# Kernel tuning notes

Hardware: AMD Instinct MI355X
Metric: run time of the kernel (lower is better)

Reference implementation:

```python
import jax, jax.numpy as jnp
import numpy as np

N = 100000      # hits
P = 512         # particle ids (0 = noise, skipped)
D = 8           # condensation-space dim
Q_MIN = 0.01
REPULSION_SCALING = 10.0


def setup_inputs() -> dict:
    key = jax.random.key(0)
    k1, k2, k3, k4, k5 = jax.random.split(key, 5)
    w = jax.random.normal(k1, (N,), dtype=jnp.float32)
    # beta in (0, 0.95) so arctanh stays well-conditioned
    beta = jax.random.uniform(k2, (N,), dtype=jnp.float32) * 0.95
    x = jax.random.normal(k3, (N, D), dtype=jnp.float32)
    y = jax.random.normal(k4, (N,), dtype=jnp.float32)
    particle_id = jax.random.randint(k5, (N,), 0, P)
    return {"w": w, "beta": beta, "x": x, "y": y, "particle_id": particle_id}


def _safe_sqrt(s):
    # sqrt with zero (sub)gradient at 0, matching torch.norm's behavior at 0
    pos = s > 0
    return jnp.where(pos, jnp.sqrt(jnp.where(pos, s, 1.0)), 0.0)


def _condensation_loss(beta, x, particle_id):
    n = beta.shape[0]
    q = jnp.arctanh(beta) ** 2 + Q_MIN                     # [N]
    # per-particle condensation point: hit with max q (torch.argmax -> first)
    q_max = jax.ops.segment_max(q, particle_id, num_segments=P)          # [P]
    counts = jax.ops.segment_sum(jnp.ones_like(q), particle_id, num_segments=P)
    is_max = q == q_max[particle_id]
    cand = jnp.where(is_max, jnp.arange(n), n)
    alpha_idx = jnp.clip(jax.ops.segment_min(cand, particle_id, num_segments=P), 0, n - 1)
    valid = (counts > 0) & (jnp.arange(P) != 0)            # skip noise pid 0 and absent pids
    q_alpha = jnp.where(valid, q_max, 0.0)                 # [P], sanitized (-inf for empty segs)
    x_alpha = x[alpha_idx]                                  # [P, D]
    # squared distances [N, P] via GEMM (avoids [N, P, D] intermediate)
    sq = (jnp.sum(x * x, axis=1, keepdims=True)
          - 2.0 * (x @ x_alpha.T)
          + jnp.sum(x_alpha * x_alpha, axis=1)[None, :])
    sq = jnp.maximum(sq, 0.0)
    dist = _safe_sqrt(sq)
    va = sq * q_alpha[None, :]                              # attractive potential
    vr = jnp.maximum(1.0 - dist, 0.0) * q_alpha[None, :]    # repulsive hinge
    M = (particle_id[:, None] == jnp.arange(P)[None, :]).astype(x.dtype)  # [N, P]
    per_p = jnp.mean(q[:, None] * (M * va + REPULSION_SCALING * (1.0 - M) * vr), axis=0)  # [P]
    return jnp.sum(jnp.where(valid, per_p, 0.0))


def reference(w, beta, x, y, particle_id):
    return _condensation_loss(beta, x, particle_id)
```

## Files before the change

kernel.cpp:

```cpp
#include <hip/hip_runtime.h>

#define P_IDS 512
#define DIM 8
#define QMIN 0.01f
#define REP 10.0f
#define CHUNK 64
#define NCHUNK (P_IDS / CHUNK)
#define HPT 4
#define HB (256 * HPT)

typedef unsigned long long ull;

__launch_bounds__(256)
__global__ void stageA_kernel(const float* __restrict__ beta,
                              const int* __restrict__ pid,
                              float* __restrict__ q_out,
                              ull* __restrict__ tables,
                              int n) {
    __shared__ ull s_keys[P_IDS];
    s_keys[threadIdx.x] = 0ULL;
    s_keys[threadIdx.x + 256] = 0ULL;
    __syncthreads();
    int i = blockIdx.x * 256 + threadIdx.x;
    if (i < n) {
        float b = beta[i];
        float at = 0.5f * logf((1.0f + b) / (1.0f - b));
        float qv = fmaf(at, at, QMIN);
        q_out[i] = qv;
        ull key = ((ull)__float_as_uint(qv) << 32) |
                  (ull)(unsigned int)(~(unsigned int)i);
        atomicMax(&s_keys[pid[i]], key);
    }
    __syncthreads();
    ull* dst = tables + (size_t)blockIdx.x * P_IDS;
    dst[threadIdx.x] = s_keys[threadIdx.x];
    dst[threadIdx.x + 256] = s_keys[threadIdx.x + 256];
}

__launch_bounds__(64)
__global__ void stageB_kernel(const ull* __restrict__ tables, int ntab,
                              const float* __restrict__ x,
                              float2* __restrict__ meta,
                              float* __restrict__ x_alpha,
                              float* __restrict__ out) {
    int p = blockIdx.x;
    ull k = 0ULL;
    for (int t = threadIdx.x; t < ntab; t += 64) {
        ull v = tables[(size_t)t * P_IDS + p];
        k = (v > k) ? v : k;
    }
#pragma unroll
    for (int off = 32; off > 0; off >>= 1) {
        ull o = __shfl_down(k, off, 64);
        k = (o > k) ? o : k;
    }
    if (threadIdx.x == 0) {
        bool valid = (k != 0ULL) && (p != 0);
        float qa = valid ? __uint_as_float((unsigned int)(k >> 32)) : 0.0f;
        int idx = valid ? (int)(~(unsigned int)(k & 0xFFFFFFFFull)) : 0;
        float4 a = ((const float4*)x)[idx * 2];
        float4 b = ((const float4*)x)[idx * 2 + 1];
        float xa2 = a.x * a.x;
        xa2 = fmaf(a.y, a.y, xa2); xa2 = fmaf(a.z, a.z, xa2); xa2 = fmaf(a.w, a.w, xa2);
        xa2 = fmaf(b.x, b.x, xa2); xa2 = fmaf(b.y, b.y, xa2); xa2 = fmaf(b.z, b.z, xa2);
        xa2 = fmaf(b.w, b.w, xa2);
        ((float4*)x_alpha)[p * 2] = a;
        ((float4*)x_alpha)[p * 2 + 1] = b;
        meta[p] = make_float2(qa, xa2);
        if (p == 0) out[0] = 0.0f;
    }
}

__launch_bounds__(256)
__global__ void loss_kernel(const float* __restrict__ x,
                            const float* __restrict__ q,
                            const int* __restrict__ pid,
                            const float2* __restrict__ meta,
                            const float* __restrict__ x_alpha,
                            float* __restrict__ out,
                            int n) {
    __shared__ float  s_xa[CHUNK * DIM];
    __shared__ float2 s_meta[CHUNK];
    int chunk = blockIdx.x & (NCHUNK - 1);
    int hb    = blockIdx.x / NCHUNK;
    int p0    = chunk * CHUNK;
    if (threadIdx.x < CHUNK * DIM / 4)
        ((float4*)s_xa)[threadIdx.x] =
            ((const float4*)(x_alpha + p0 * DIM))[threadIdx.x];
    if (threadIdx.x < CHUNK) s_meta[threadIdx.x] = meta[p0 + threadIdx.x];
    __syncthreads();

    float xi[HPT][DIM], xi2[HPT], qi[HPT], acc[HPT];
    int   myj[HPT];
    int base = hb * HB + threadIdx.x;
#pragma unroll
    for (int h = 0; h < HPT; ++h) {
        int i = base + h * 256;
        bool act = i < n;
        int ii = act ? i : 0;
        float4 v0 = ((const float4*)x)[ii * 2];
        float4 v1 = ((const float4*)x)[ii * 2 + 1];
        xi[h][0] = v0.x; xi[h][1] = v0.y; xi[h][2] = v0.z; xi[h][3] = v0.w;
        xi[h][4] = v1.x; xi[h][5] = v1.y; xi[h][6] = v1.z; xi[h][7] = v1.w;
        float s = 0.0f;
#pragma unroll
        for (int d = 0; d < DIM; ++d) s = fmaf(xi[h][d], xi[h][d], s);
        xi2[h] = s;
        qi[h]  = act ? q[ii] : 0.0f;
        myj[h] = act ? (pid[ii] - p0) : -1;
        acc[h] = 0.0f;
    }

    for (int j = 0; j < CHUNK; ++j) {
        float2 m  = s_meta[j];
        float4 a0 = ((const float4*)s_xa)[j * 2];
        float4 a1 = ((const float4*)s_xa)[j * 2 + 1];
        float sq[HPT];
#pragma unroll
        for (int h = 0; h < HPT; ++h) {
            float dot = xi[h][0] * a0.x;
            dot = fmaf(xi[h][1], a0.y, dot); dot = fmaf(xi[h][2], a0.z, dot);
            dot = fmaf(xi[h][3], a0.w, dot); dot = fmaf(xi[h][4], a1.x, dot);
            dot = fmaf(xi[h][5], a1.y, dot); dot = fmaf(xi[h][6], a1.z, dot);
            dot = fmaf(xi[h][7], a1.w, dot);
            sq[h] = fmaxf(fmaf(-2.0f, dot, xi2[h] + m.y), 0.0f);
        }
        float mn = fminf(fminf(sq[0], sq[1]), fminf(sq[2], sq[3]));
        if (__any(mn < 1.0f)) {
#pragma unroll
            for (int h = 0; h < HPT; ++h) {
                float vr = fmaxf(1.0f - __builtin_amdgcn_sqrtf(sq[h]), 0.0f);
                acc[h] = fmaf(vr, m.x, acc[h]);
            }
        }
    }

    float partial = 0.0f;
#pragma unroll
    for (int h = 0; h < HPT; ++h) {
        float t = REP * acc[h];
        int j = myj[h];
        if (j >= 0 && j < CHUNK) {
            float2 m = s_meta[j];
            float dot = xi[h][0] * s_xa[j * DIM + 0];
#pragma unroll
            for (int d = 1; d < DIM; ++d) dot = fmaf(xi[h][d], s_xa[j * DIM + d], dot);
            float sq = fmaxf(fmaf(-2.0f, dot, xi2[h] + m.y), 0.0f);
            float vr = fmaxf(1.0f - __builtin_amdgcn_sqrtf(sq), 0.0f);
            t += m.x * (sq - REP * vr);
        }
        partial = fmaf(qi[h], t, partial);
    }

#pragma unroll
    for (int off = 32; off > 0; off >>= 1)
        partial += __shfl_down(partial, off, 64);
    __shared__ float s_red[4];
    if ((threadIdx.x & 63) == 0) s_red[threadIdx.x >> 6] = partial;
    __syncthreads();
    if (threadIdx.x == 0)
        atomicAdd(out, (s_red[0] + s_red[1] + s_red[2] + s_red[3]) / (float)n);
}

extern "C" void kernel_launch(void* const* d_in, const int* in_sizes, int n_in,
                              void* d_out, int out_size, void* d_ws, size_t ws_size,
                              hipStream_t stream) {
    int n = in_sizes[0];
    const float* beta = (const float*)d_in[1];
    const float* x    = (const float*)d_in[2];
    const int*   pid  = (const int*)d_in[4];
    float* out = (float*)d_out;

    int a_blocks = (n + 255) / 256;
    char* ws = (char*)d_ws;
    size_t tab_bytes = (size_t)a_blocks * P_IDS * sizeof(ull);
    tab_bytes = (tab_bytes + 255) & ~(size_t)255;
    size_t q_bytes = (((size_t)n * 4) + 255) & ~(size_t)255;
    ull*    tables  = (ull*)ws;
    float*  q       = (float*)(ws + tab_bytes);
    float2* meta    = (float2*)(ws + tab_bytes + q_bytes);
    float*  x_alpha = (float*)(ws + tab_bytes + q_bytes + P_IDS * sizeof(float2));

    stageA_kernel<<<a_blocks, 256, 0, stream>>>(beta, pid, q, tables, n);
    stageB_kernel<<<P_IDS, 64, 0, stream>>>(tables, a_blocks, x, meta, x_alpha, out);
    int hit_blocks = (n + HB - 1) / HB;
    loss_kernel<<<hit_blocks * NCHUNK, 256, 0, stream>>>(x, q, pid, meta, x_alpha, out, n);
}
```

Measured before the change: 96.58 us.

## Fuse three stages into one cooperative kernel with grid-wide syncs

```diff
diff --git a/kernel.cpp b/kernel.cpp
--- a/kernel.cpp
+++ b/kernel.cpp
@@ -1,4 +1,7 @@
 #include <hip/hip_runtime.h>
+#include <hip/hip_cooperative_groups.h>
+
+namespace cg = cooperative_groups;
 
 #define P_IDS 512
 #define DIM 8
@@ -11,155 +14,164 @@
 
 typedef unsigned long long ull;
 
-__launch_bounds__(256)
-__global__ void stageA_kernel(const float* __restrict__ beta,
-                              const int* __restrict__ pid,
-                              float* __restrict__ q_out,
-                              ull* __restrict__ tables,
-                              int n) {
-    __shared__ ull s_keys[P_IDS];
-    s_keys[threadIdx.x] = 0ULL;
-    s_keys[threadIdx.x + 256] = 0ULL;
-    __syncthreads();
-    int i = blockIdx.x * 256 + threadIdx.x;
-    if (i < n) {
-        float b = beta[i];
-        float at = 0.5f * logf((1.0f + b) / (1.0f - b));
-        float qv = fmaf(at, at, QMIN);
-        q_out[i] = qv;
-        ull key = ((ull)__float_as_uint(qv) << 32) |
-                  (ull)(unsigned int)(~(unsigned int)i);
-        atomicMax(&s_keys[pid[i]], key);
-    }
-    __syncthreads();
-    ull* dst = tables + (size_t)blockIdx.x * P_IDS;
-    dst[threadIdx.x] = s_keys[threadIdx.x];
-    dst[threadIdx.x + 256] = s_keys[threadIdx.x + 256];
-}
-
-__launch_bounds__(64)
-__global__ void stageB_kernel(const ull* __restrict__ tables, int ntab,
-                              const float* __restrict__ x,
-                              float2* __restrict__ meta,
-                              float* __restrict__ x_alpha,
-                              float* __restrict__ out) {
-    int p = blockIdx.x;
-    ull k = 0ULL;
-    for (int t = threadIdx.x; t < ntab; t += 64) {
-        ull v = tables[(size_t)t * P_IDS + p];
-        k = (v > k) ? v : k;
-    }
-#pragma unroll
-    for (int off = 32; off > 0; off >>= 1) {
-        ull o = __shfl_down(k, off, 64);
-        k = (o > k) ? o : k;
-    }
-    if (threadIdx.x == 0) {
-        bool valid = (k != 0ULL) && (p != 0);
-        float qa = valid ? __uint_as_float((unsigned int)(k >> 32)) : 0.0f;
-        int idx = valid ? (int)(~(unsigned int)(k & 0xFFFFFFFFull)) : 0;
-        float4 a = ((const float4*)x)[idx * 2];
-        float4 b = ((const float4*)x)[idx * 2 + 1];
-        float xa2 = a.x * a.x;
-        xa2 = fmaf(a.y, a.y, xa2); xa2 = fmaf(a.z, a.z, xa2); xa2 = fmaf(a.w, a.w, xa2);
-        xa2 = fmaf(b.x, b.x, xa2); xa2 = fmaf(b.y, b.y, xa2); xa2 = fmaf(b.z, b.z, xa2);
-        xa2 = fmaf(b.w, b.w, xa2);
-        ((float4*)x_alpha)[p * 2] = a;
-        ((float4*)x_alpha)[p * 2 + 1] = b;
-        meta[p] = make_float2(qa, xa2);
-        if (p == 0) out[0] = 0.0f;
-    }
-}
-
-__launch_bounds__(256)
-__global__ void loss_kernel(const float* __restrict__ x,
-                            const float* __restrict__ q,
-                            const int* __restrict__ pid,
-                            const float2* __restrict__ meta,
-                            const float* __restrict__ x_alpha,
-                            float* __restrict__ out,
-                            int n) {
+__launch_bounds__(256, 4)
+__global__ void fused_kernel(const float* __restrict__ beta,
+                             const float* __restrict__ x,
+                             const int* __restrict__ pid,
+                             float* __restrict__ q,
+                             ull* __restrict__ tables,
+                             float2* __restrict__ meta,
+                             float* __restrict__ x_alpha,
+                             float* __restrict__ out,
+                             int n, int a_blocks, int tiles) {
+    cg::grid_group grid = cg::this_grid();
+    __shared__ ull    s_keys[P_IDS];
+    __shared__ ull    s_kred[4];
     __shared__ float  s_xa[CHUNK * DIM];
     __shared__ float2 s_meta[CHUNK];
-    int chunk = blockIdx.x & (NCHUNK - 1);
-    int hb    = blockIdx.x / NCHUNK;
-    int p0    = chunk * CHUNK;
-    if (threadIdx.x < CHUNK * DIM / 4)
-        ((float4*)s_xa)[threadIdx.x] =
-            ((const float4*)(x_alpha + p0 * DIM))[threadIdx.x];
-    if (threadIdx.x < CHUNK) s_meta[threadIdx.x] = meta[p0 + threadIdx.x];
-    __syncthreads();
-
-    float xi[HPT][DIM], xi2[HPT], qi[HPT], acc[HPT];
-    int   myj[HPT];
-    int base = hb * HB + threadIdx.x;
-#pragma unroll
-    for (int h = 0; h < HPT; ++h) {
-        int i = base + h * 256;
-        bool act = i < n;
-        int ii = act ? i : 0;
-        float4 v0 = ((const float4*)x)[ii * 2];
-        float4 v1 = ((const float4*)x)[ii * 2 + 1];
-        xi[h][0] = v0.x; xi[h][1] = v0.y; xi[h][2] = v0.z; xi[h][3] = v0.w;
-        xi[h][4] = v1.x; xi[h][5] = v1.y; xi[h][6] = v1.z; xi[h][7] = v1.w;
-        float s = 0.0f;
-#pragma unroll
-        for (int d = 0; d < DIM; ++d) s = fmaf(xi[h][d], xi[h][d], s);
-        xi2[h] = s;
-        qi[h]  = act ? q[ii] : 0.0f;
-        myj[h] = act ? (pid[ii] - p0) : -1;
-        acc[h] = 0.0f;
+    __shared__ float  s_red[4];
+
+    const int b   = blockIdx.x;
+    const int tid = threadIdx.x;
+
+    if (b < a_blocks) {
+        s_keys[tid] = 0ULL;
+        s_keys[tid + 256] = 0ULL;
+        __syncthreads();
+        int i = b * 256 + tid;
+        if (i < n) {
+            float bt = beta[i];
+            float at = 0.5f * logf((1.0f + bt) / (1.0f - bt));
+            float qv = fmaf(at, at, QMIN);
+            q[i] = qv;
+            ull key = ((ull)__float_as_uint(qv) << 32) |
+                      (ull)(unsigned int)(~(unsigned int)i);
+            atomicMax(&s_keys[pid[i]], key);
+        }
+        __syncthreads();
+        ull* dst = tables + (size_t)b * P_IDS;
+        dst[tid] = s_keys[tid];
+        dst[tid + 256] = s_keys[tid + 256];
     }
-
-    for (int j = 0; j < CHUNK; ++j) {
-        float2 m  = s_meta[j];
-        float4 a0 = ((const float4*)s_xa)[j * 2];
-        float4 a1 = ((const float4*)s_xa)[j * 2 + 1];
-        float sq[HPT];
+    grid.sync();
+
+    if (b < P_IDS) {
+        int p = b;
+        ull k = 0ULL;
+        for (int t = tid; t < a_blocks; t += 256) {
+            ull v = tables[(size_t)t * P_IDS + p];
+            k = (v > k) ? v : k;
+        }
+#pragma unroll
+        for (int off = 32; off > 0; off >>= 1) {
+            ull o = __shfl_down(k, off, 64);
+            k = (o > k) ? o : k;
+        }
+        if ((tid & 63) == 0) s_kred[tid >> 6] = k;
+        __syncthreads();
+        if (tid == 0) {
+            k = s_kred[0];
+            k = (s_kred[1] > k) ? s_kred[1] : k;
+            k = (s_kred[2] > k) ? s_kred[2] : k;
+            k = (s_kred[3] > k) ? s_kred[3] : k;
+            bool valid = (k != 0ULL) && (p != 0);
+            float qa = valid ? __uint_as_float((unsigned int)(k >> 32)) : 0.0f;
+            int idx = valid ? (int)(~(unsigned int)(k & 0xFFFFFFFFull)) : 0;
+            float4 a0 = ((const float4*)x)[idx * 2];
+            float4 a1 = ((const float4*)x)[idx * 2 + 1];
+            float xa2 = a0.x * a0.x;
+            xa2 = fmaf(a0.y, a0.y, xa2); xa2 = fmaf(a0.z, a0.z, xa2);
+            xa2 = fmaf(a0.w, a0.w, xa2); xa2 = fmaf(a1.x, a1.x, xa2);
+            xa2 = fmaf(a1.y, a1.y, xa2); xa2 = fmaf(a1.z, a1.z, xa2);
+            xa2 = fmaf(a1.w, a1.w, xa2);
+            ((float4*)x_alpha)[p * 2] = a0;
+            ((float4*)x_alpha)[p * 2 + 1] = a1;
+            meta[p] = make_float2(qa, xa2);
+            if (p == 0) out[0] = 0.0f;
+        }
+    }
+    grid.sync();
+
+    if (b < tiles) {
+        int chunk = b & (NCHUNK - 1);
+        int hb    = b / NCHUNK;
+        int p0    = chunk * CHUNK;
+        if (tid < CHUNK * DIM / 4)
+            ((float4*)s_xa)[tid] = ((const float4*)(x_alpha + p0 * DIM))[tid];
+        if (tid < CHUNK) s_meta[tid] = meta[p0 + tid];
+        __syncthreads();
+
+        float xi[HPT][DIM], xi2[HPT], qi[HPT], acc[HPT];
+        int   myj[HPT];
+        int base = hb * HB + tid;
 #pragma unroll
         for (int h = 0; h < HPT; ++h) {
-            float dot = xi[h][0] * a0.x;
-            dot = fmaf(xi[h][1], a0.y, dot); dot = fmaf(xi[h][2], a0.z, dot);
-            dot = fmaf(xi[h][3], a0.w, dot); dot = fmaf(xi[h][4], a1.x, dot);
-            dot = fmaf(xi[h][5], a1.y, dot); dot = fmaf(xi[h][6], a1.z, dot);
-            dot = fmaf(xi[h][7], a1.w, dot);
-            sq[h] = fmaxf(fmaf(-2.0f, dot, xi2[h] + m.y), 0.0f);
-        }
-        float mn = fminf(fminf(sq[0], sq[1]), fminf(sq[2], sq[3]));
-        if (__any(mn < 1.0f)) {
+            int i = base + h * 256;
+            bool act = i < n;
+            int ii = act ? i : 0;
+            float4 v0 = ((const float4*)x)[ii * 2];
+            float4 v1 = ((const float4*)x)[ii * 2 + 1];
+            xi[h][0] = v0.x; xi[h][1] = v0.y; xi[h][2] = v0.z; xi[h][3] = v0.w;
+            xi[h][4] = v1.x; xi[h][5] = v1.y; xi[h][6] = v1.z; xi[h][7] = v1.w;
+            float s = 0.0f;
+#pragma unroll
+            for (int d = 0; d < DIM; ++d) s = fmaf(xi[h][d], xi[h][d], s);
+            xi2[h] = s;
+            qi[h]  = act ? q[ii] : 0.0f;
+            myj[h] = act ? (pid[ii] - p0) : -1;
+            acc[h] = 0.0f;
+        }
+
+        for (int j = 0; j < CHUNK; ++j) {
+            float2 m  = s_meta[j];
+            float4 a0 = ((const float4*)s_xa)[j * 2];
+            float4 a1 = ((const float4*)s_xa)[j * 2 + 1];
+            float sq[HPT];
 #pragma unroll
             for (int h = 0; h < HPT; ++h) {
-                float vr = fmaxf(1.0f - __builtin_amdgcn_sqrtf(sq[h]), 0.0f);
-                acc[h] = fmaf(vr, m.x, acc[h]);
+                float dot = xi[h][0] * a0.x;
+                dot = fmaf(xi[h][1], a0.y, dot); dot = fmaf(xi[h][2], a0.z, dot);
+                dot = fmaf(xi[h][3], a0.w, dot); dot = fmaf(xi[h][4], a1.x, dot);
+                dot = fmaf(xi[h][5], a1.y, dot); dot = fmaf(xi[h][6], a1.z, dot);
+                dot = fmaf(xi[h][7], a1.w, dot);
+                sq[h] = fmaxf(fmaf(-2.0f, dot, xi2[h] + m.y), 0.0f);
             }
-        }
+            float mn = fminf(fminf(sq[0], sq[1]), fminf(sq[2], sq[3]));
+            if (__any(mn < 1.0f)) {
+#pragma unroll
+                for (int h = 0; h < HPT; ++h) {
+                    float vr = fmaxf(1.0f - __builtin_amdgcn_sqrtf(sq[h]), 0.0f);
+                    acc[h] = fmaf(vr, m.x, acc[h]);
+                }
+            }
+        }
+
+        float partial = 0.0f;
+#pragma unroll
+        for (int h = 0; h < HPT; ++h) {
+            float t = REP * acc[h];
+            int j = myj[h];
+            if (j >= 0 && j < CHUNK) {
+                float2 m = s_meta[j];
+                float dot = xi[h][0] * s_xa[j * DIM + 0];
+#pragma unroll
+                for (int d = 1; d < DIM; ++d)
+                    dot = fmaf(xi[h][d], s_xa[j * DIM + d], dot);
+                float sq = fmaxf(fmaf(-2.0f, dot, xi2[h] + m.y), 0.0f);
+                float vr = fmaxf(1.0f - __builtin_amdgcn_sqrtf(sq), 0.0f);
+                t += m.x * (sq - REP * vr);
+            }
+            partial = fmaf(qi[h], t, partial);
+        }
+
+#pragma unroll
+        for (int off = 32; off > 0; off >>= 1)
+            partial += __shfl_down(partial, off, 64);
+        if ((tid & 63) == 0) s_red[tid >> 6] = partial;
+        __syncthreads();
+        if (tid == 0)
+            atomicAdd(out, (s_red[0] + s_red[1] + s_red[2] + s_red[3]) / (float)n);
     }
-
-    float partial = 0.0f;
-#pragma unroll
-    for (int h = 0; h < HPT; ++h) {
-        float t = REP * acc[h];
-        int j = myj[h];
-        if (j >= 0 && j < CHUNK) {
-            float2 m = s_meta[j];
-            float dot = xi[h][0] * s_xa[j * DIM + 0];
-#pragma unroll
-            for (int d = 1; d < DIM; ++d) dot = fmaf(xi[h][d], s_xa[j * DIM + d], dot);
-            float sq = fmaxf(fmaf(-2.0f, dot, xi2[h] + m.y), 0.0f);
-            float vr = fmaxf(1.0f - __builtin_amdgcn_sqrtf(sq), 0.0f);
-            t += m.x * (sq - REP * vr);
-        }
-        partial = fmaf(qi[h], t, partial);
-    }
-
-#pragma unroll
-    for (int off = 32; off > 0; off >>= 1)
-        partial += __shfl_down(partial, off, 64);
-    __shared__ float s_red[4];
-    if ((threadIdx.x & 63) == 0) s_red[threadIdx.x >> 6] = partial;
-    __syncthreads();
-    if (threadIdx.x == 0)
-        atomicAdd(out, (s_red[0] + s_red[1] + s_red[2] + s_red[3]) / (float)n);
 }
 
 extern "C" void kernel_launch(void* const* d_in, const int* in_sizes, int n_in,
@@ -172,17 +184,21 @@
     float* out = (float*)d_out;
 
     int a_blocks = (n + 255) / 256;
+    int tiles    = ((n + HB - 1) / HB) * NCHUNK;
+    int grid     = tiles > P_IDS ? tiles : P_IDS;
+    if (grid < a_blocks) grid = a_blocks;
+
     char* ws = (char*)d_ws;
-    size_t tab_bytes = (size_t)a_blocks * P_IDS * sizeof(ull);
-    tab_bytes = (tab_bytes + 255) & ~(size_t)255;
-    size_t q_bytes = (((size_t)n * 4) + 255) & ~(size_t)255;
+    size_t tab_bytes = ((size_t)a_blocks * P_IDS * sizeof(ull) + 255) & ~(size_t)255;
+    size_t q_bytes   = (((size_t)n * 4) + 255) & ~(size_t)255;
     ull*    tables  = (ull*)ws;
     float*  q       = (float*)(ws + tab_bytes);
     float2* meta    = (float2*)(ws + tab_bytes + q_bytes);
     float*  x_alpha = (float*)(ws + tab_bytes + q_bytes + P_IDS * sizeof(float2));
 
-    stageA_kernel<<<a_blocks, 256, 0, stream>>>(beta, pid, q, tables, n);
-    stageB_kernel<<<P_IDS, 64, 0, stream>>>(tables, a_blocks, x, meta, x_alpha, out);
-    int hit_blocks = (n + HB - 1) / HB;
-    loss_kernel<<<hit_blocks * NCHUNK, 256, 0, stream>>>(x, q, pid, meta, x_alpha, out, n);
+    void* args[] = {(void*)&beta, (void*)&x, (void*)&pid, (void*)&q,
+                    (void*)&tables, (void*)&meta, (void*)&x_alpha, (void*)&out,
+                    (void*)&n, (void*)&a_blocks, (void*)&tiles};
+    hipLaunchCooperativeKernel((void*)fused_kernel, dim3(grid), dim3(256),
+                               args, 0, stream);
 }
```

Measured after the change: 285.7 us. 196% more time.

## Fold per-particle argmax reduction into loss kernel with fixed 64 partial tables

Applied to the files above, without the earlier changes.

```diff
diff --git a/kernel.cpp b/kernel.cpp
--- a/kernel.cpp
+++ b/kernel.cpp
@@ -4,6 +4,7 @@
 #define DIM 8
 #define QMIN 0.01f
 #define REP 10.0f
+#define TBLS 64
 #define CHUNK 64
 #define NCHUNK (P_IDS / CHUNK)
 #define HPT 4
@@ -16,13 +17,13 @@
                               const int* __restrict__ pid,
                               float* __restrict__ q_out,
                               ull* __restrict__ tables,
+                              float* __restrict__ out,
                               int n) {
     __shared__ ull s_keys[P_IDS];
     s_keys[threadIdx.x] = 0ULL;
     s_keys[threadIdx.x + 256] = 0ULL;
     __syncthreads();
-    int i = blockIdx.x * 256 + threadIdx.x;
-    if (i < n) {
+    for (int i = blockIdx.x * 256 + threadIdx.x; i < n; i += TBLS * 256) {
         float b = beta[i];
         float at = 0.5f * logf((1.0f + b) / (1.0f - b));
         float qv = fmaf(at, at, QMIN);
@@ -35,64 +36,58 @@
     ull* dst = tables + (size_t)blockIdx.x * P_IDS;
     dst[threadIdx.x] = s_keys[threadIdx.x];
     dst[threadIdx.x + 256] = s_keys[threadIdx.x + 256];
-}
-
-__launch_bounds__(64)
-__global__ void stageB_kernel(const ull* __restrict__ tables, int ntab,
-                              const float* __restrict__ x,
-                              float2* __restrict__ meta,
-                              float* __restrict__ x_alpha,
-                              float* __restrict__ out) {
-    int p = blockIdx.x;
-    ull k = 0ULL;
-    for (int t = threadIdx.x; t < ntab; t += 64) {
-        ull v = tables[(size_t)t * P_IDS + p];
-        k = (v > k) ? v : k;
-    }
-#pragma unroll
-    for (int off = 32; off > 0; off >>= 1) {
-        ull o = __shfl_down(k, off, 64);
-        k = (o > k) ? o : k;
-    }
-    if (threadIdx.x == 0) {
-        bool valid = (k != 0ULL) && (p != 0);
-        float qa = valid ? __uint_as_float((unsigned int)(k >> 32)) : 0.0f;
-        int idx = valid ? (int)(~(unsigned int)(k & 0xFFFFFFFFull)) : 0;
-        float4 a = ((const float4*)x)[idx * 2];
-        float4 b = ((const float4*)x)[idx * 2 + 1];
-        float xa2 = a.x * a.x;
-        xa2 = fmaf(a.y, a.y, xa2); xa2 = fmaf(a.z, a.z, xa2); xa2 = fmaf(a.w, a.w, xa2);
-        xa2 = fmaf(b.x, b.x, xa2); xa2 = fmaf(b.y, b.y, xa2); xa2 = fmaf(b.z, b.z, xa2);
-        xa2 = fmaf(b.w, b.w, xa2);
-        ((float4*)x_alpha)[p * 2] = a;
-        ((float4*)x_alpha)[p * 2 + 1] = b;
-        meta[p] = make_float2(qa, xa2);
-        if (p == 0) out[0] = 0.0f;
-    }
+    if (blockIdx.x == 0 && threadIdx.x == 0) out[0] = 0.0f;
 }
 
 __launch_bounds__(256)
 __global__ void loss_kernel(const float* __restrict__ x,
                             const float* __restrict__ q,
                             const int* __restrict__ pid,
-                            const float2* __restrict__ meta,
-                            const float* __restrict__ x_alpha,
+                            const ull* __restrict__ tables,
                             float* __restrict__ out,
                             int n) {
+    __shared__ ull    s_part[4][CHUNK];
     __shared__ float  s_xa[CHUNK * DIM];
     __shared__ float2 s_meta[CHUNK];
-    int chunk = blockIdx.x & (NCHUNK - 1);
-    int hb    = blockIdx.x / NCHUNK;
-    int p0    = chunk * CHUNK;
-    if (threadIdx.x < CHUNK * DIM / 4)
-        ((float4*)s_xa)[threadIdx.x] =
-            ((const float4*)(x_alpha + p0 * DIM))[threadIdx.x];
-    if (threadIdx.x < CHUNK) s_meta[threadIdx.x] = meta[p0 + threadIdx.x];
+    __shared__ float  s_red[4];
+
+    const int tid  = threadIdx.x;
+    const int wave = tid >> 6, lane = tid & 63;
+    const int chunk = blockIdx.x & (NCHUNK - 1);
+    const int hb    = blockIdx.x / NCHUNK;
+    const int p0    = chunk * CHUNK;
+
+    ull k = 0ULL;
+#pragma unroll
+    for (int t = wave; t < TBLS; t += 4) {
+        ull v = tables[(size_t)t * P_IDS + p0 + lane];
+        k = (v > k) ? v : k;
+    }
+    s_part[wave][lane] = k;
+    __syncthreads();
+    if (tid < CHUNK) {
+        k = s_part[0][tid];
+        ull v1 = s_part[1][tid], v2 = s_part[2][tid], v3 = s_part[3][tid];
+        k = (v1 > k) ? v1 : k; k = (v2 > k) ? v2 : k; k = (v3 > k) ? v3 : k;
+        bool valid = (k != 0ULL) && ((p0 + tid) != 0);
+        float qa = valid ? __uint_as_float((unsigned int)(k >> 32)) : 0.0f;
+        int idx = valid ? (int)(~(unsigned int)(k & 0xFFFFFFFFull)) : 0;
+        float4 a0 = ((const float4*)x)[idx * 2];
+        float4 a1 = ((const float4*)x)[idx * 2 + 1];
+        float xa2 = a0.x * a0.x;
+        xa2 = fmaf(a0.y, a0.y, xa2); xa2 = fmaf(a0.z, a0.z, xa2);
+        xa2 = fmaf(a0.w, a0.w, xa2); xa2 = fmaf(a1.x, a1.x, xa2);
+        xa2 = fmaf(a1.y, a1.y, xa2); xa2 = fmaf(a1.z, a1.z, xa2);
+        xa2 = fmaf(a1.w, a1.w, xa2);
+        ((float4*)s_xa)[tid * 2] = a0;
+        ((float4*)s_xa)[tid * 2 + 1] = a1;
+        s_meta[tid] = make_float2(qa, xa2);
+    }
     __syncthreads();
 
     float xi[HPT][DIM], xi2[HPT], qi[HPT], acc[HPT];
     int   myj[HPT];
-    int base = hb * HB + threadIdx.x;
+    int base = hb * HB + tid;
 #pragma unroll
     for (int h = 0; h < HPT; ++h) {
         int i = base + h * 256;
@@ -144,7 +139,8 @@
             float2 m = s_meta[j];
             float dot = xi[h][0] * s_xa[j * DIM + 0];
 #pragma unroll
-            for (int d = 1; d < DIM; ++d) dot = fmaf(xi[h][d], s_xa[j * DIM + d], dot);
+            for (int d = 1; d < DIM; ++d)
+                dot = fmaf(xi[h][d], s_xa[j * DIM + d], dot);
             float sq = fmaxf(fmaf(-2.0f, dot, xi2[h] + m.y), 0.0f);
             float vr = fmaxf(1.0f - __builtin_amdgcn_sqrtf(sq), 0.0f);
             t += m.x * (sq - REP * vr);
@@ -155,10 +151,9 @@
 #pragma unroll
     for (int off = 32; off > 0; off >>= 1)
         partial += __shfl_down(partial, off, 64);
-    __shared__ float s_red[4];
-    if ((threadIdx.x & 63) == 0) s_red[threadIdx.x >> 6] = partial;
+    if ((tid & 63) == 0) s_red[tid >> 6] = partial;
     __syncthreads();
-    if (threadIdx.x == 0)
+    if (tid == 0)
         atomicAdd(out, (s_red[0] + s_red[1] + s_red[2] + s_red[3]) / (float)n);
 }
 
@@ -171,18 +166,12 @@
     const int*   pid  = (const int*)d_in[4];
     float* out = (float*)d_out;
 
-    int a_blocks = (n + 255) / 256;
     char* ws = (char*)d_ws;
-    size_t tab_bytes = (size_t)a_blocks * P_IDS * sizeof(ull);
-    tab_bytes = (tab_bytes + 255) & ~(size_t)255;
-    size_t q_bytes = (((size_t)n * 4) + 255) & ~(size_t)255;
-    ull*    tables  = (ull*)ws;
-    float*  q       = (float*)(ws + tab_bytes);
-    float2* meta    = (float2*)(ws + tab_bytes + q_bytes);
-    float*  x_alpha = (float*)(ws + tab_bytes + q_bytes + P_IDS * sizeof(float2));
+    size_t tab_bytes = ((size_t)TBLS * P_IDS * sizeof(ull) + 255) & ~(size_t)255;
+    ull*   tables = (ull*)ws;
+    float* q      = (float*)(ws + tab_bytes);
 
-    stageA_kernel<<<a_blocks, 256, 0, stream>>>(beta, pid, q, tables, n);
-    stageB_kernel<<<P_IDS, 64, 0, stream>>>(tables, a_blocks, x, meta, x_alpha, out);
+    stageA_kernel<<<TBLS, 256, 0, stream>>>(beta, pid, q, tables, out, n);
     int hit_blocks = (n + HB - 1) / HB;
-    loss_kernel<<<hit_blocks * NCHUNK, 256, 0, stream>>>(x, q, pid, meta, x_alpha, out, n);
+    loss_kernel<<<hit_blocks * NCHUNK, 256, 0, stream>>>(x, q, pid, tables, out, n);
 }
```

New measurement: 97.61 us. No clear change (+1.1%).
